# Kernel optimization log

Hardware: AMD Instinct MI355X
Metric: run time of the kernel (lower is better)

## Reference

```python
import jax, jax.numpy as jnp
import numpy as np

N_NODES = 100000


def gcn_conv(x, W, b, src, dst, norm, n_nodes):
    # x: [N, F_in] -> [N, F_out]; GCNConv: D^-1/2 (A+I) D^-1/2 (X W) + b
    h = x @ W                                   # [N, F_out]
    msg = h[src] * norm[:, None]                # [E+N, F_out] gather + scale
    out = jax.ops.segment_sum(msg, dst, num_segments=n_nodes)  # scatter-add
    return out + b


def setup_inputs() -> dict:
    key = jax.random.key(0)
    k0, k1, k2, k3, k4, k5 = jax.random.split(key, 6)
    n, e, f_in, f_hid, n_cls = N_NODES, 1600000, 128, 128, 3
    x = jax.random.normal(k0, (n, f_in), dtype=jnp.float32)
    edge_index = jax.random.randint(k1, (2, e), 0, n, dtype=jnp.int64)
    s1 = 1.0 / np.sqrt(f_in)
    s2 = 1.0 / np.sqrt(f_hid)
    W1 = jax.random.uniform(k2, (f_in, f_hid), jnp.float32, -s1, s1)
    b1 = jnp.zeros((f_hid,), jnp.float32)
    W2 = jax.random.uniform(k3, (f_hid, f_hid), jnp.float32, -s2, s2)
    b2 = jnp.zeros((f_hid,), jnp.float32)
    Wfc = jax.random.uniform(k4, (f_hid, n_cls), jnp.float32, -s2, s2)
    bfc = jax.random.uniform(k5, (n_cls,), jnp.float32, -s2, s2)
    return {"x": x, "edge_index": edge_index, "W1": W1, "b1": b1,
            "W2": W2, "b2": b2, "Wfc": Wfc, "bfc": bfc}


def reference(x, edge_index, W1, b1, W2, b2, Wfc, bfc):
    n = x.shape[0]
    # add self-loops (PyG GCNConv default add_self_loops=True)
    loops = jnp.arange(n, dtype=edge_index.dtype)
    src = jnp.concatenate([edge_index[0], loops])
    dst = jnp.concatenate([edge_index[1], loops])
    deg = jax.ops.segment_sum(jnp.ones_like(dst, dtype=x.dtype), dst,
                              num_segments=n)
    dinv = jax.lax.rsqrt(deg)                   # deg >= 1 due to self-loops
    norm = dinv[src] * dinv[dst]                # [E+N]
    h = jax.nn.relu(gcn_conv(x, W1, b1, src, dst, norm, n))   # dropout=eval id
    h = jax.nn.relu(gcn_conv(h, W2, b2, src, dst, norm, n))
    return jnp.tanh(h @ Wfc + bfc)              # [N, 3]
```

## Files before the change

kernel.cpp:

```cpp
#include <hip/hip_runtime.h>
#include <hip/hip_bf16.h>
#include <hip/hip_fp16.h>


#define NODE_F 128

typedef __attribute__((ext_vector_type(8))) short bf16x8;
typedef __attribute__((ext_vector_type(8))) unsigned short u16x8;
typedef __attribute__((ext_vector_type(4))) float f32x4;

__device__ inline unsigned short bf16_rn(float x) {
    unsigned u = __builtin_bit_cast(unsigned, x);
    unsigned r = (u + 0x7fffu + ((u >> 16) & 1u)) >> 16;
    return (unsigned short)r;
}
__device__ inline float bf16_to_f(unsigned short h) {
    unsigned u = (unsigned)h << 16;
    return __builtin_bit_cast(float, u);
}
__device__ inline void acc4_h(float a[4], uint2 v) {
    __half2 h01 = __builtin_bit_cast(__half2, v.x);
    __half2 h23 = __builtin_bit_cast(__half2, v.y);
    float2 f01 = __half22float2(h01), f23 = __half22float2(h23);
    a[0] += f01.x; a[1] += f01.y; a[2] += f23.x; a[3] += f23.y;
}


__global__ __launch_bounds__(256) void wconv_kernel(const float* __restrict__ W1,
                                                    const float* __restrict__ W2,
                                                    unsigned short* __restrict__ WhiT,
                                                    unsigned short* __restrict__ WloT)
{
    const float* W = blockIdx.x ? W2 : W1;
    unsigned short* hiT = WhiT + blockIdx.x * 128 * 128;
    unsigned short* loT = WloT + blockIdx.x * 128 * 128;
    int tid = threadIdx.x;
    for (int i = tid; i < 128 * 128; i += 256) {
        int k = i >> 7, n = i & 127;
        float x = W[i];
        unsigned short hi = bf16_rn(x);
        float lo = x - bf16_to_f(hi);
        hiT[n * 128 + k] = hi;
        loT[n * 128 + k] = bf16_rn(lo);
    }
}


__global__ __launch_bounds__(256) void scan_block_kernel(
    const int* __restrict__ degE, int* __restrict__ row_start,
    int* __restrict__ bsum, int N)
{
    __shared__ int s[256];
    const int tid = threadIdx.x;
    const int idx = blockIdx.x * 1024 + tid * 4;
    int v0 = (idx + 0 < N) ? degE[idx + 0] : 0;
    int v1 = (idx + 1 < N) ? degE[idx + 1] : 0;
    int v2 = (idx + 2 < N) ? degE[idx + 2] : 0;
    int v3 = (idx + 3 < N) ? degE[idx + 3] : 0;
    int t = v0 + v1 + v2 + v3;
    s[tid] = t;
    __syncthreads();
    #pragma unroll
    for (int off = 1; off < 256; off <<= 1) {
        int x = (tid >= off) ? s[tid - off] : 0;
        __syncthreads();
        s[tid] += x;
        __syncthreads();
    }
    int excl = s[tid] - t;
    if (idx + 0 < N) row_start[idx + 0] = excl;
    if (idx + 1 < N) row_start[idx + 1] = excl + v0;
    if (idx + 2 < N) row_start[idx + 2] = excl + v0 + v1;
    if (idx + 3 < N) row_start[idx + 3] = excl + v0 + v1 + v2;
    if (tid == 255) bsum[blockIdx.x] = s[255];
}

__global__ __launch_bounds__(1024) void scan_tops_kernel(int* __restrict__ bsum, int nb) {
    __shared__ int s[1024];
    const int tid = threadIdx.x;
    int v = (tid < nb) ? bsum[tid] : 0;
    s[tid] = v;
    __syncthreads();
    #pragma unroll
    for (int off = 1; off < 1024; off <<= 1) {
        int x = (tid >= off) ? s[tid - off] : 0;
        __syncthreads();
        s[tid] += x;
        __syncthreads();
    }
    if (tid < nb) bsum[tid] = s[tid] - v;
}

__global__ void scan_finish_kernel(const int* __restrict__ degE, int* __restrict__ row_start,
                                   const int* __restrict__ bsum, float* __restrict__ dinv, int N)
{
    int i = blockIdx.x * blockDim.x + threadIdx.x;
    if (i >= N) return;
    int rs = row_start[i] + bsum[i >> 10];
    row_start[i] = rs;
    dinv[i] = rsqrtf((float)degE[i] + 1.0f);
    if (i == N - 1) row_start[N] = rs + degE[i];
}


template<bool SPLIT_IN, bool SCALE_OUT>
__device__ __forceinline__ void gemm_body(
    const float* __restrict__ Xf,
    const unsigned short* __restrict__ Xhi_g, const unsigned short* __restrict__ Xlo_g,
    const unsigned short* __restrict__ WhiT, const unsigned short* __restrict__ WloT,
    const float* __restrict__ dinv,
    __half* __restrict__ Hout, int N, int bid,
    unsigned short* xhi, unsigned short* xlo)
{
    const int tid  = threadIdx.x;
    const int lane = tid & 63;
    const int w    = tid >> 6;
    const int rbase = bid * 64;

    bf16x8 bhi[2][4], blo[2][4];
    {
        int n0   = w * 32 + (lane & 15);
        int koct = (lane >> 4) * 8;
        #pragma unroll
        for (int nt = 0; nt < 2; ++nt) {
            #pragma unroll
            for (int kk = 0; kk < 4; ++kk) {
                size_t o = (size_t)(n0 + nt * 16) * 128 + kk * 32 + koct;
                bhi[nt][kk] = *reinterpret_cast<const bf16x8*>(WhiT + o);
                blo[nt][kk] = *reinterpret_cast<const bf16x8*>(WloT + o);
            }
        }
    }

    if (!SPLIT_IN) {
        #pragma unroll
        for (int it = 0; it < 8; ++it) {
            int f   = it * 256 + tid;
            int row = f >> 5;
            int k4  = f & 31;
            float4 v = make_float4(0.f, 0.f, 0.f, 0.f);
            if (rbase + row < N)
                v = *reinterpret_cast<const float4*>(Xf + (size_t)(rbase + row) * NODE_F + k4 * 4);
            float xs[4] = {v.x, v.y, v.z, v.w};
            ushort4 h4, l4;
            unsigned short* hp = &h4.x;
            unsigned short* lp = &l4.x;
            #pragma unroll
            for (int j = 0; j < 4; ++j) {
                unsigned short hi = bf16_rn(xs[j]);
                hp[j] = hi;
                lp[j] = bf16_rn(xs[j] - bf16_to_f(hi));
            }
            int byte = row * 256 + ((k4 * 8) ^ ((row & 7) << 4));
            *reinterpret_cast<ushort4*>(reinterpret_cast<char*>(xhi) + byte) = h4;
            *reinterpret_cast<ushort4*>(reinterpret_cast<char*>(xlo) + byte) = l4;
        }
    } else {
        #pragma unroll
        for (int it = 0; it < 4; ++it) {
            int idx = it * 256 + tid;
            int row = idx >> 4;
            int k8  = idx & 15;
            u16x8 h = {0, 0, 0, 0, 0, 0, 0, 0};
            u16x8 l = {0, 0, 0, 0, 0, 0, 0, 0};
            if (rbase + row < N) {
                size_t g = (size_t)(rbase + row) * NODE_F + k8 * 8;
                h = *reinterpret_cast<const u16x8*>(Xhi_g + g);
                l = *reinterpret_cast<const u16x8*>(Xlo_g + g);
            }
            int byte = row * 256 + ((k8 * 16) ^ ((row & 7) << 4));
            *reinterpret_cast<u16x8*>(reinterpret_cast<char*>(xhi) + byte) = h;
            *reinterpret_cast<u16x8*>(reinterpret_cast<char*>(xlo) + byte) = l;
        }
    }
    __syncthreads();

    f32x4 acc[4][2];
    #pragma unroll
    for (int m = 0; m < 4; ++m)
        #pragma unroll
        for (int nt = 0; nt < 2; ++nt)
            acc[m][nt] = (f32x4){0.f, 0.f, 0.f, 0.f};

    #pragma unroll
    for (int kk = 0; kk < 4; ++kk) {
        #pragma unroll
        for (int m = 0; m < 4; ++m) {
            int row  = m * 16 + (lane & 15);
            int koff = kk * 64 + (lane >> 4) * 16;
            int byte = row * 256 + (koff ^ ((row & 7) << 4));
            bf16x8 ahi = *reinterpret_cast<const bf16x8*>(reinterpret_cast<char*>(xhi) + byte);
            bf16x8 alo = *reinterpret_cast<const bf16x8*>(reinterpret_cast<char*>(xlo) + byte);
            #pragma unroll
            for (int nt = 0; nt < 2; ++nt) {
                acc[m][nt] = __builtin_amdgcn_mfma_f32_16x16x32_bf16(ahi, bhi[nt][kk], acc[m][nt], 0, 0, 0);
                acc[m][nt] = __builtin_amdgcn_mfma_f32_16x16x32_bf16(ahi, blo[nt][kk], acc[m][nt], 0, 0, 0);
                acc[m][nt] = __builtin_amdgcn_mfma_f32_16x16x32_bf16(alo, bhi[nt][kk], acc[m][nt], 0, 0, 0);
            }
        }
    }

    #pragma unroll
    for (int m = 0; m < 4; ++m) {
        int row = rbase + m * 16 + (lane >> 4) * 4;
        int col = w * 32 + (lane & 15);
        #pragma unroll
        for (int nt = 0; nt < 2; ++nt) {
            #pragma unroll
            for (int r = 0; r < 4; ++r) {
                if (row + r < N) {
                    float v = acc[m][nt][r];
                    if (SCALE_OUT) v *= dinv[row + r];
                    Hout[(size_t)(row + r) * NODE_F + col + nt * 16] = __float2half(v);
                }
            }
        }
    }
}


__global__ __launch_bounds__(256) void gemm1deg_kernel(
    const int* __restrict__ dst, int* __restrict__ degE, int* __restrict__ rank, int E,
    int total_threads,
    const float* __restrict__ X, const unsigned short* __restrict__ WhiT,
    const unsigned short* __restrict__ WloT, __half* __restrict__ H, int N)
{
    __shared__ unsigned short xhi[64 * 128];
    __shared__ unsigned short xlo[64 * 128];
    for (int e = blockIdx.x * 256 + threadIdx.x; e < E; e += total_threads)
        rank[e] = atomicAdd(&degE[dst[e]], 1);
    gemm_body<false, false>(X, nullptr, nullptr, WhiT, WloT, nullptr,
                            H, N, blockIdx.x, xhi, xlo);
}


__global__ __launch_bounds__(256) void hybridB_kernel(
    const int* __restrict__ src, const int* __restrict__ dst,
    const int* __restrict__ rank, const int* __restrict__ row_start,
    int* __restrict__ csr_src, int E, int fill_blocks,
    __half* __restrict__ H, const int* __restrict__ degE, int N)
{
    if ((int)blockIdx.x < fill_blocks) {
        int e = blockIdx.x * 256 + threadIdx.x;
        if (e < E) csr_src[row_start[dst[e]] + rank[e]] = src[e];
    } else {
        int idx = (blockIdx.x - fill_blocks) * 256 + threadIdx.x;
        if (idx < N * 16) {
            int row = idx >> 4;
            float ds = rsqrtf((float)degE[row] + 1.0f);
            __half2* p = reinterpret_cast<__half2*>(H) + (size_t)idx * 4;
            #pragma unroll
            for (int j = 0; j < 4; ++j) {
                float2 v = __half22float2(p[j]);
                v.x *= ds; v.y *= ds;
                p[j] = __float22half2_rn(v);
            }
        }
    }
}


__device__ __forceinline__ void gather_core(
    const __half* __restrict__ Hs, const int* __restrict__ csr_src,
    const int* __restrict__ row_start, int node, int li, int h, float a[4])
{
    const char* Hb = reinterpret_cast<const char*>(Hs);
    a[0] = a[1] = a[2] = a[3] = 0.f;
    if (h == 0)
        acc4_h(a, *reinterpret_cast<const uint2*>(Hb + ((size_t)node * 256 + li * 8)));

    int i   = row_start[node];
    int end = row_start[node + 1];
    for (; i + 7 < end; i += 8) {
        int s0 = csr_src[i + 0 + h];
        int s1 = csr_src[i + 2 + h];
        int s2 = csr_src[i + 4 + h];
        int s3 = csr_src[i + 6 + h];
        uint2 v0 = *reinterpret_cast<const uint2*>(Hb + ((size_t)s0 * 256 + li * 8));
        uint2 v1 = *reinterpret_cast<const uint2*>(Hb + ((size_t)s1 * 256 + li * 8));
        uint2 v2 = *reinterpret_cast<const uint2*>(Hb + ((size_t)s2 * 256 + li * 8));
        uint2 v3 = *reinterpret_cast<const uint2*>(Hb + ((size_t)s3 * 256 + li * 8));
        acc4_h(a, v0); acc4_h(a, v1); acc4_h(a, v2); acc4_h(a, v3);
    }
    for (; i + 1 < end; i += 2) {
        int s = csr_src[i + h];
        acc4_h(a, *reinterpret_cast<const uint2*>(Hb + ((size_t)s * 256 + li * 8)));
    }
    if (i < end && h == 0) {
        int s = csr_src[i];
        acc4_h(a, *reinterpret_cast<const uint2*>(Hb + ((size_t)s * 256 + li * 8)));
    }
    #pragma unroll
    for (int j = 0; j < 4; ++j)
        a[j] += __shfl_xor(a[j], 32);
}


__global__ __launch_bounds__(256) void gather1_kernel(
    const __half* __restrict__ Hs, const int* __restrict__ csr_src,
    const int* __restrict__ row_start, const float* __restrict__ dinv,
    const float* __restrict__ b,
    unsigned short* __restrict__ Xhi, unsigned short* __restrict__ Xlo, int N)
{
    int node = (blockIdx.x * blockDim.x + threadIdx.x) >> 6;
    int lane = threadIdx.x & 63;
    int li = lane & 31, h = lane >> 5;
    if (node >= N) return;

    float a[4];
    gather_core(Hs, csr_src, row_start, node, li, h, a);

    if (h == 0) {
        const float dd = dinv[node];
        float4 bb = *reinterpret_cast<const float4*>(b + li * 4);
        float r0 = fmaxf(bb.x + dd * a[0], 0.f);
        float r1 = fmaxf(bb.y + dd * a[1], 0.f);
        float r2 = fmaxf(bb.z + dd * a[2], 0.f);
        float r3 = fmaxf(bb.w + dd * a[3], 0.f);
        ushort4 h4, l4;
        h4.x = bf16_rn(r0); l4.x = bf16_rn(r0 - bf16_to_f(h4.x));
        h4.y = bf16_rn(r1); l4.y = bf16_rn(r1 - bf16_to_f(h4.y));
        h4.z = bf16_rn(r2); l4.z = bf16_rn(r2 - bf16_to_f(h4.z));
        h4.w = bf16_rn(r3); l4.w = bf16_rn(r3 - bf16_to_f(h4.w));
        *reinterpret_cast<ushort4*>(Xhi + (size_t)node * NODE_F + li * 4) = h4;
        *reinterpret_cast<ushort4*>(Xlo + (size_t)node * NODE_F + li * 4) = l4;
    }
}


__global__ __launch_bounds__(256) void gather2fc_kernel(
    const __half* __restrict__ Hs, const int* __restrict__ csr_src,
    const int* __restrict__ row_start, const float* __restrict__ dinv,
    const float* __restrict__ b, const float* __restrict__ Wfc,
    const float* __restrict__ bfc, float* __restrict__ out, int N)
{
    int node = (blockIdx.x * blockDim.x + threadIdx.x) >> 6;
    int lane = threadIdx.x & 63;
    int li = lane & 31, h = lane >> 5;
    if (node >= N) return;

    float a[4];
    gather_core(Hs, csr_src, row_start, node, li, h, a);

    const float dd = dinv[node];
    float4 bb = *reinterpret_cast<const float4*>(b + li * 4);
    float bv[4] = {bb.x, bb.y, bb.z, bb.w};
    float p0 = 0.f, p1 = 0.f, p2 = 0.f;
    #pragma unroll
    for (int j = 0; j < 4; ++j) {
        float r = fmaxf(bv[j] + dd * a[j], 0.f);
        const float* wr = Wfc + (size_t)(li * 4 + j) * 3;
        p0 += r * wr[0]; p1 += r * wr[1]; p2 += r * wr[2];
    }
    #pragma unroll
    for (int off = 16; off > 0; off >>= 1) {
        p0 += __shfl_down(p0, off);
        p1 += __shfl_down(p1, off);
        p2 += __shfl_down(p2, off);
    }
    if (lane == 0) {
        out[(size_t)node * 3 + 0] = tanhf(p0 + bfc[0]);
        out[(size_t)node * 3 + 1] = tanhf(p1 + bfc[1]);
        out[(size_t)node * 3 + 2] = tanhf(p2 + bfc[2]);
    }
}


__global__ __launch_bounds__(256) void gemm2_kernel(
    const unsigned short* __restrict__ Xhi_g, const unsigned short* __restrict__ Xlo_g,
    const unsigned short* __restrict__ WhiT, const unsigned short* __restrict__ WloT,
    const float* __restrict__ dinv, __half* __restrict__ Hs, int N)
{
    __shared__ unsigned short xhi[64 * 128];
    __shared__ unsigned short xlo[64 * 128];
    gemm_body<true, true>(nullptr, Xhi_g, Xlo_g, WhiT, WloT, dinv,
                          Hs, N, blockIdx.x, xhi, xlo);
}

extern "C" void kernel_launch(void* const* d_in, const int* in_sizes, int n_in,
                              void* d_out, int out_size, void* d_ws, size_t ws_size,
                              hipStream_t stream)
{
    const float* x    = (const float*)d_in[0];
    const int*   edge = (const int*)d_in[1];
    const float* W1   = (const float*)d_in[2];
    const float* b1   = (const float*)d_in[3];
    const float* W2   = (const float*)d_in[4];
    const float* b2   = (const float*)d_in[5];
    const float* Wfc  = (const float*)d_in[6];
    const float* bfc  = (const float*)d_in[7];
    float* out = (float*)d_out;

    const int N = in_sizes[0] / NODE_F;
    const int E = in_sizes[1] / 2;
    const int* src = edge;
    const int* dst = edge + E;

    char* ws = (char*)d_ws;
    size_t off = 0;
    auto alloc = [&](size_t bytes) {
        void* p = ws + off;
        off += (bytes + 511) & ~511ull;
        return p;
    };
    const int nblk1024 = (N + 1023) / 1024;
    float* dinv      = (float*)alloc((size_t)N * 4);
    int*   degE      = (int*)  alloc((size_t)N * 4);
    int*   rank      = (int*)  alloc((size_t)E * 4);
    int*   row_start = (int*)  alloc((size_t)(N + 1) * 4);
    int*   bsum      = (int*)  alloc((size_t)nblk1024 * 4);
    int*   csr_src   = (int*)  alloc((size_t)E * 4);
    unsigned short* WhiT = (unsigned short*)alloc(2 * 128 * 128 * 2);
    unsigned short* WloT = (unsigned short*)alloc(2 * 128 * 128 * 2);
    __half* Hs       = (__half*)alloc((size_t)N * NODE_F * 2);
    unsigned short* Xhi = (unsigned short*)alloc((size_t)N * NODE_F * 2);
    unsigned short* Xlo = (unsigned short*)alloc((size_t)N * NODE_F * 2);
    (void)ws_size; (void)n_in; (void)out_size;

    const int B = 256;
    const int gemm_grid   = (N + 63) / 64;
    const int edge_grid   = (E + B - 1) / B;
    const int scale_grid  = (N * 16 + B - 1) / B;
    const int gather_grid = (N + 3) / 4;

    wconv_kernel<<<2, B, 0, stream>>>(W1, W2, WhiT, WloT);
    hipMemsetAsync(degE, 0, (size_t)N * 4, stream);

    gemm1deg_kernel<<<gemm_grid, B, 0, stream>>>(
        dst, degE, rank, E, gemm_grid * B, x, WhiT, WloT, Hs, N);

    scan_block_kernel<<<nblk1024, B, 0, stream>>>(degE, row_start, bsum, N);
    scan_tops_kernel<<<1, 1024, 0, stream>>>(bsum, nblk1024);
    scan_finish_kernel<<<(N + B - 1) / B, B, 0, stream>>>(degE, row_start, bsum, dinv, N);

    hybridB_kernel<<<edge_grid + scale_grid, B, 0, stream>>>(
        src, dst, rank, row_start, csr_src, E, edge_grid, Hs, degE, N);

    gather1_kernel<<<gather_grid, B, 0, stream>>>(Hs, csr_src, row_start, dinv, b1, Xhi, Xlo, N);

    gemm2_kernel<<<gemm_grid, B, 0, stream>>>(Xhi, Xlo, WhiT + 128 * 128, WloT + 128 * 128,
                                              dinv, Hs, N);

    gather2fc_kernel<<<gather_grid, B, 0, stream>>>(Hs, csr_src, row_start, dinv, b2,
                                                    Wfc, bfc, out, N);
}
```

Measured before the change: 336.0 us.

## Widen gather loads to 16B per lane and split degree counting into dedicated blocks

The gather kernels now give each lane 8 fp16 features through 16-byte loads, so 16 lanes cover one 256-byte row and four edge slots are processed in parallel per wave. The partial sums are combined with two xor-shuffles. Separately, the fused GEMM1 and degree kernel no longer has every block run both the atomic degree counting and the GEMM tile. It interleaves blocks so one in five does only the edge atomics and the other four do the GEMM. The aim is fewer, wider memory transactions in the gather and less serialization inside the fused kernel, at the cost of more registers and shuffles per lane.

```diff
diff --git a/kernel.cpp b/kernel.cpp
--- a/kernel.cpp
+++ b/kernel.cpp
@@ -18,11 +18,14 @@
     unsigned u = (unsigned)h << 16;
     return __builtin_bit_cast(float, u);
 }
-__device__ inline void acc4_h(float a[4], uint2 v) {
-    __half2 h01 = __builtin_bit_cast(__half2, v.x);
-    __half2 h23 = __builtin_bit_cast(__half2, v.y);
-    float2 f01 = __half22float2(h01), f23 = __half22float2(h23);
-    a[0] += f01.x; a[1] += f01.y; a[2] += f23.x; a[3] += f23.y;
+__device__ inline void acc8_h(float a[8], uint4 v) {
+    unsigned vv[4] = {v.x, v.y, v.z, v.w};
+    #pragma unroll
+    for (int j = 0; j < 4; ++j) {
+        float2 f = __half22float2(__builtin_bit_cast(__half2, vv[j]));
+        a[2 * j]     += f.x;
+        a[2 * j + 1] += f.y;
+    }
 }
 
 
@@ -221,16 +224,23 @@
 
 __global__ __launch_bounds__(256) void gemm1deg_kernel(
     const int* __restrict__ dst, int* __restrict__ degE, int* __restrict__ rank, int E,
-    int total_threads,
+    int edge_blocks, int gemm_blocks,
     const float* __restrict__ X, const unsigned short* __restrict__ WhiT,
     const unsigned short* __restrict__ WloT, __half* __restrict__ H, int N)
 {
     __shared__ unsigned short xhi[64 * 128];
     __shared__ unsigned short xlo[64 * 128];
-    for (int e = blockIdx.x * 256 + threadIdx.x; e < E; e += total_threads)
-        rank[e] = atomicAdd(&degE[dst[e]], 1);
-    gemm_body<false, false>(X, nullptr, nullptr, WhiT, WloT, nullptr,
-                            H, N, blockIdx.x, xhi, xlo);
+    int q = blockIdx.x / 5, r = blockIdx.x % 5;
+    if (r == 4) {
+        int stride = edge_blocks * 256;
+        for (int e = q * 256 + threadIdx.x; e < E; e += stride)
+            rank[e] = atomicAdd(&degE[dst[e]], 1);
+    } else {
+        int gid = q * 4 + r;
+        if (gid < gemm_blocks)
+            gemm_body<false, false>(X, nullptr, nullptr, WhiT, WloT, nullptr,
+                                    H, N, gid, xhi, xlo);
+    }
 }
 
 
@@ -262,37 +272,35 @@
 
 __device__ __forceinline__ void gather_core(
     const __half* __restrict__ Hs, const int* __restrict__ csr_src,
-    const int* __restrict__ row_start, int node, int li, int h, float a[4])
+    const int* __restrict__ row_start, int node, int ql, int qi, float a[8])
 {
     const char* Hb = reinterpret_cast<const char*>(Hs);
-    a[0] = a[1] = a[2] = a[3] = 0.f;
-    if (h == 0)
-        acc4_h(a, *reinterpret_cast<const uint2*>(Hb + ((size_t)node * 256 + li * 8)));
+    #pragma unroll
+    for (int j = 0; j < 8; ++j) a[j] = 0.f;
+    if (qi == 0)
+        acc8_h(a, *reinterpret_cast<const uint4*>(Hb + ((size_t)node * 256 + ql * 16)));
 
     int i   = row_start[node];
     int end = row_start[node + 1];
     for (; i + 7 < end; i += 8) {
-        int s0 = csr_src[i + 0 + h];
-        int s1 = csr_src[i + 2 + h];
-        int s2 = csr_src[i + 4 + h];
-        int s3 = csr_src[i + 6 + h];
-        uint2 v0 = *reinterpret_cast<const uint2*>(Hb + ((size_t)s0 * 256 + li * 8));
-        uint2 v1 = *reinterpret_cast<const uint2*>(Hb + ((size_t)s1 * 256 + li * 8));
-        uint2 v2 = *reinterpret_cast<const uint2*>(Hb + ((size_t)s2 * 256 + li * 8));
-        uint2 v3 = *reinterpret_cast<const uint2*>(Hb + ((size_t)s3 * 256 + li * 8));
-        acc4_h(a, v0); acc4_h(a, v1); acc4_h(a, v2); acc4_h(a, v3);
-    }
-    for (; i + 1 < end; i += 2) {
-        int s = csr_src[i + h];
-        acc4_h(a, *reinterpret_cast<const uint2*>(Hb + ((size_t)s * 256 + li * 8)));
-    }
-    if (i < end && h == 0) {
-        int s = csr_src[i];
-        acc4_h(a, *reinterpret_cast<const uint2*>(Hb + ((size_t)s * 256 + li * 8)));
-    }
-    #pragma unroll
-    for (int j = 0; j < 4; ++j)
+        int s0 = csr_src[i + qi];
+        int s1 = csr_src[i + 4 + qi];
+        uint4 v0 = *reinterpret_cast<const uint4*>(Hb + ((size_t)s0 * 256 + ql * 16));
+        uint4 v1 = *reinterpret_cast<const uint4*>(Hb + ((size_t)s1 * 256 + ql * 16));
+        acc8_h(a, v0);
+        acc8_h(a, v1);
+    }
+    for (; i < end; i += 4) {
+        if (i + qi < end) {
+            int s = csr_src[i + qi];
+            acc8_h(a, *reinterpret_cast<const uint4*>(Hb + ((size_t)s * 256 + ql * 16)));
+        }
+    }
+    #pragma unroll
+    for (int j = 0; j < 8; ++j) {
         a[j] += __shfl_xor(a[j], 32);
+        a[j] += __shfl_xor(a[j], 16);
+    }
 }
 
 
@@ -304,26 +312,24 @@
 {
     int node = (blockIdx.x * blockDim.x + threadIdx.x) >> 6;
     int lane = threadIdx.x & 63;
-    int li = lane & 31, h = lane >> 5;
+    int ql = lane & 15, qi = lane >> 4;
     if (node >= N) return;
 
-    float a[4];
-    gather_core(Hs, csr_src, row_start, node, li, h, a);
-
-    if (h == 0) {
+    float a[8];
+    gather_core(Hs, csr_src, row_start, node, ql, qi, a);
+
+    if (qi == 0) {
         const float dd = dinv[node];
-        float4 bb = *reinterpret_cast<const float4*>(b + li * 4);
-        float r0 = fmaxf(bb.x + dd * a[0], 0.f);
-        float r1 = fmaxf(bb.y + dd * a[1], 0.f);
-        float r2 = fmaxf(bb.z + dd * a[2], 0.f);
-        float r3 = fmaxf(bb.w + dd * a[3], 0.f);
-        ushort4 h4, l4;
-        h4.x = bf16_rn(r0); l4.x = bf16_rn(r0 - bf16_to_f(h4.x));
-        h4.y = bf16_rn(r1); l4.y = bf16_rn(r1 - bf16_to_f(h4.y));
-        h4.z = bf16_rn(r2); l4.z = bf16_rn(r2 - bf16_to_f(h4.z));
-        h4.w = bf16_rn(r3); l4.w = bf16_rn(r3 - bf16_to_f(h4.w));
-        *reinterpret_cast<ushort4*>(Xhi + (size_t)node * NODE_F + li * 4) = h4;
-        *reinterpret_cast<ushort4*>(Xlo + (size_t)node * NODE_F + li * 4) = l4;
+        u16x8 h8, l8;
+        #pragma unroll
+        for (int j = 0; j < 8; ++j) {
+            float r = fmaxf(b[ql * 8 + j] + dd * a[j], 0.f);
+            unsigned short hi = bf16_rn(r);
+            h8[j] = hi;
+            l8[j] = bf16_rn(r - bf16_to_f(hi));
+        }
+        *reinterpret_cast<u16x8*>(Xhi + (size_t)node * NODE_F + ql * 8) = h8;
+        *reinterpret_cast<u16x8*>(Xlo + (size_t)node * NODE_F + ql * 8) = l8;
     }
 }
 
@@ -336,24 +342,22 @@
 {
     int node = (blockIdx.x * blockDim.x + threadIdx.x) >> 6;
     int lane = threadIdx.x & 63;
-    int li = lane & 31, h = lane >> 5;
+    int ql = lane & 15, qi = lane >> 4;
     if (node >= N) return;
 
-    float a[4];
-    gather_core(Hs, csr_src, row_start, node, li, h, a);
+    float a[8];
+    gather_core(Hs, csr_src, row_start, node, ql, qi, a);
 
     const float dd = dinv[node];
-    float4 bb = *reinterpret_cast<const float4*>(b + li * 4);
-    float bv[4] = {bb.x, bb.y, bb.z, bb.w};
     float p0 = 0.f, p1 = 0.f, p2 = 0.f;
     #pragma unroll
-    for (int j = 0; j < 4; ++j) {
-        float r = fmaxf(bv[j] + dd * a[j], 0.f);
-        const float* wr = Wfc + (size_t)(li * 4 + j) * 3;
+    for (int j = 0; j < 8; ++j) {
+        float r = fmaxf(b[ql * 8 + j] + dd * a[j], 0.f);
+        const float* wr = Wfc + (size_t)(ql * 8 + j) * 3;
         p0 += r * wr[0]; p1 += r * wr[1]; p2 += r * wr[2];
     }
     #pragma unroll
-    for (int off = 16; off > 0; off >>= 1) {
+    for (int off = 8; off > 0; off >>= 1) {
         p0 += __shfl_down(p0, off);
         p1 += __shfl_down(p1, off);
         p2 += __shfl_down(p2, off);
@@ -423,11 +427,14 @@
     const int scale_grid  = (N * 16 + B - 1) / B;
     const int gather_grid = (N + 3) / 4;
 
+    const int edge_blocks  = (gemm_grid + 3) / 4;
+    const int total_blocks = gemm_grid + edge_blocks + 4;
+
     wconv_kernel<<<2, B, 0, stream>>>(W1, W2, WhiT, WloT);
     hipMemsetAsync(degE, 0, (size_t)N * 4, stream);
 
-    gemm1deg_kernel<<<gemm_grid, B, 0, stream>>>(
-        dst, degE, rank, E, gemm_grid * B, x, WhiT, WloT, Hs, N);
+    gemm1deg_kernel<<<total_blocks, B, 0, stream>>>(
+        dst, degE, rank, E, edge_blocks, gemm_grid, x, WhiT, WloT, Hs, N);
 
     scan_block_kernel<<<nblk1024, B, 0, stream>>>(degE, row_start, bsum, N);
     scan_tops_kernel<<<1, 1024, 0, stream>>>(bsum, nblk1024);
```

Result: faster. 320.8 us (-4.5%).
